# Performance work log

Hardware: AMD Instinct MI355X
Metric: run time of the kernel (lower is better)

The kernel has to match this reference:

```python
import jax, jax.numpy as jnp
import numpy as np

NEG_INF = -1e9  # masked similarity sentinel (cosine sims are in [-1, 1])
EPS = 1e-12     # matches torch F.normalize eps


def _l2norm(x, axis=-1):
    n = jnp.linalg.norm(x, axis=axis, keepdims=True)
    return x / jnp.maximum(n, EPS)


def setup_inputs() -> dict:
    key = jax.random.key(0)
    k1, k2, k3, k4 = jax.random.split(key, 4)
    B, R, D, N = 16, 29, 512, 20000
    query_visual_features = jax.random.normal(k1, (B, R, D), dtype=jnp.float32)
    kb_features = jax.random.normal(k2, (R, N, D), dtype=jnp.float32)
    query_image_ids = jax.random.randint(k3, (B,), 0, 100000)
    kb_image_ids = jax.random.randint(k4, (R, N), 0, 100000)
    return {
        "query_visual_features": query_visual_features,
        "kb_features": kb_features,
        "query_image_ids": query_image_ids,
        "kb_image_ids": kb_image_ids,
        "top_k": 5,
    }


def reference(query_visual_features, kb_features, query_image_ids, kb_image_ids, top_k):
    # Normalize queries (F.normalize dim=2) and KB entries (normalized at init).
    q = _l2norm(query_visual_features)          # [B, R, D]
    kb = _l2norm(kb_features)                   # [R, N, D]
    # Per-sample, per-region cosine similarity against that region's candidates.
    sim = jnp.einsum("brd,rnd->brn", q, kb)    # [B, R, N]
    # Exclude candidates coming from the same image as the query.
    same = kb_image_ids[None, :, :] == query_image_ids[:, None, None]  # [B, R, N]
    sim = jnp.where(same, NEG_INF, sim)
    top_vals, top_idx = jax.lax.top_k(sim, top_k)  # [B, R, k]
    # similarity_scores in the original = best (top-1) similarity per region.
    similarity_scores = top_vals[..., 0]            # [B, R]
    return similarity_scores, top_vals, top_idx
```

## Files before the change

### kernel.cpp

```cpp
#include <hip/hip_runtime.h>
#include <stddef.h>
#include <stdint.h>

#define B_ 16
#define R_ 29
#define D_ 512
#define DF4 128
#define N_ 20000
#define K_ 5
#define TILE 128
#define NTIX ((N_ + TILE - 1) / TILE)
#define NG (NTIX * 4)
#define PCAND (NG * K_)
#define NEG_MASK (-1.0e9f)
#define SENT (-3.0e38f)
#define IXMAX 0x7fffffff

__global__ __launch_bounds__(64) void knorm_kernel(const float* __restrict__ q,
                                                   float* __restrict__ qn) {
    int pair = blockIdx.x;
    int b = pair / R_;
    int r = pair % R_;
    int lane = threadIdx.x;
    const float4* src = (const float4*)(q + ((size_t)(b * R_ + r)) * D_);
    float4 x0 = src[lane * 2];
    float4 x1 = src[lane * 2 + 1];
    float ss = x0.x * x0.x + x0.y * x0.y + x0.z * x0.z + x0.w * x0.w +
               x1.x * x1.x + x1.y * x1.y + x1.z * x1.z + x1.w * x1.w;
#pragma unroll
    for (int off = 32; off; off >>= 1) ss += __shfl_xor(ss, off);
    float inv = 1.0f / fmaxf(sqrtf(ss), 1e-12f);
    float4 y0, y1;
    y0.x = x0.x * inv; y0.y = x0.y * inv; y0.z = x0.z * inv; y0.w = x0.w * inv;
    y1.x = x1.x * inv; y1.y = x1.y * inv; y1.z = x1.z * inv; y1.w = x1.w * inv;
    float4* dst = (float4*)(qn + ((size_t)(r * B_ + b)) * D_);
    dst[lane * 2] = y0;
    dst[lane * 2 + 1] = y1;
}

__global__ __launch_bounds__(256) void ksim_kernel(const float* __restrict__ kb,
                                                   const float* __restrict__ qn,
                                                   const int* __restrict__ qid,
                                                   const int* __restrict__ kbid,
                                                   float* __restrict__ pvals,
                                                   int* __restrict__ pidx) {
    __shared__ float4 qs[B_ * DF4];
    const int r = blockIdx.y;
    const int n0 = blockIdx.x * TILE;
    const int tid = threadIdx.x;

    {
        const float4* src = (const float4*)(qn + (size_t)r * B_ * D_);
#pragma unroll
        for (int i = 0; i < 32; ++i) qs[tid + 256 * i] = src[tid + 256 * i];
    }
    __syncthreads();

    const int w = tid >> 6;
    const int lane = tid & 63;
    const int g = lane >> 3;
    const int s = lane & 7;

    int rowi[4];
    const float4* rowp[4];
    float acc[4][B_];
    float nrm[4];
#pragma unroll
    for (int m = 0; m < 4; ++m) {
        rowi[m] = n0 + w * 32 + g + m * 8;
        int rc = rowi[m] < N_ ? rowi[m] : N_ - 1;
        rowp[m] = (const float4*)(kb + (size_t)r * N_ * D_ + (size_t)rc * D_) + s;
        nrm[m] = 0.0f;
#pragma unroll
        for (int b = 0; b < B_; ++b) acc[m][b] = 0.0f;
    }

    float4 kv[4], kn[4];
#pragma unroll
    for (int m = 0; m < 4; ++m) kv[m] = rowp[m][0];

    for (int p = 0; p < 16; ++p) {
        if (p < 15) {
#pragma unroll
            for (int m = 0; m < 4; ++m) kn[m] = rowp[m][(p + 1) * 8];
        }
#pragma unroll
        for (int m = 0; m < 4; ++m)
            nrm[m] += kv[m].x * kv[m].x + kv[m].y * kv[m].y +
                      kv[m].z * kv[m].z + kv[m].w * kv[m].w;
#pragma unroll
        for (int b = 0; b < B_; ++b) {
            const float4 qv = qs[b * DF4 + p * 8 + s];
#pragma unroll
            for (int m = 0; m < 4; ++m)
                acc[m][b] += kv[m].x * qv.x + kv[m].y * qv.y +
                             kv[m].z * qv.z + kv[m].w * qv.w;
        }
#pragma unroll
        for (int m = 0; m < 4; ++m) kv[m] = kn[m];
    }

#pragma unroll
    for (int m = 0; m < 4; ++m) {
        nrm[m] += __shfl_xor(nrm[m], 1);
        nrm[m] += __shfl_xor(nrm[m], 2);
        nrm[m] += __shfl_xor(nrm[m], 4);
#pragma unroll
        for (int b = 0; b < B_; ++b) {
            acc[m][b] += __shfl_xor(acc[m][b], 1);
            acc[m][b] += __shfl_xor(acc[m][b], 2);
            acc[m][b] += __shfl_xor(acc[m][b], 4);
        }
    }

    float rinv[4];
    int myid[4];
#pragma unroll
    for (int m = 0; m < 4; ++m) {
        rinv[m] = 1.0f / fmaxf(sqrtf(nrm[m]), 1e-12f);
        myid[m] = (rowi[m] < N_) ? kbid[(size_t)r * N_ + rowi[m]] : -1;
    }

    const int group = blockIdx.x * 4 + w;
    for (int b = 0; b < B_; ++b) {
        const int qb = qid[b];
        float v[4];
#pragma unroll
        for (int m = 0; m < 4; ++m) {
            float sv = acc[m][b] * rinv[m];
            if (myid[m] == qb) sv = NEG_MASK;
            if (rowi[m] >= N_) sv = SENT;
            v[m] = sv;
        }
        for (int k = 0; k < K_; ++k) {
            float bv = v[0];
            int bx = rowi[0];
#pragma unroll
            for (int m = 1; m < 4; ++m)
                if (v[m] > bv || (v[m] == bv && rowi[m] < bx)) { bv = v[m]; bx = rowi[m]; }
#pragma unroll
            for (int off = 8; off < 64; off <<= 1) {
                float ov = __shfl_xor(bv, off);
                int ox = __shfl_xor(bx, off);
                if (ov > bv || (ov == bv && ox < bx)) { bv = ov; bx = ox; }
            }
            if (lane == 0) {
                size_t o = (((size_t)r * B_ + b) * NG + group) * K_ + k;
                pvals[o] = bv;
                pidx[o] = bx;
            }
#pragma unroll
            for (int m = 0; m < 4; ++m)
                if (rowi[m] == bx) v[m] = SENT;
        }
    }
}

__global__ __launch_bounds__(64) void ktop_kernel(const float* __restrict__ pvals,
                                                  const int* __restrict__ pidx,
                                                  float* __restrict__ out) {
    int pair = blockIdx.x;
    int b = pair / R_;
    int r = pair % R_;
    int lane = threadIdx.x;
    const float* pv = pvals + ((size_t)r * B_ + b) * PCAND;
    const int* px = pidx + ((size_t)r * B_ + b) * PCAND;

    float tv[5];
    int tx[5];
#pragma unroll
    for (int t = 0; t < 5; ++t) { tv[t] = SENT; tx[t] = IXMAX; }

    for (int j = 0; j < (PCAND + 63) / 64; ++j) {
        int c = lane + 64 * j;
        if (c < PCAND) {
            float v = pv[c];
            int ix = px[c];
            if (v > tv[4] || (v == tv[4] && ix < tx[4])) {
                tv[4] = v; tx[4] = ix;
#pragma unroll
                for (int t = 4; t > 0; --t)
                    if (tv[t] > tv[t - 1] ||
                        (tv[t] == tv[t - 1] && tx[t] < tx[t - 1])) {
                        float fv = tv[t]; tv[t] = tv[t - 1]; tv[t - 1] = fv;
                        int fx = tx[t]; tx[t] = tx[t - 1]; tx[t - 1] = fx;
                    }
            }
        }
    }

#pragma unroll
    for (int k = 0; k < K_; ++k) {
        float bv = tv[0];
        int bx = tx[0];
#pragma unroll
        for (int off = 32; off; off >>= 1) {
            float ov = __shfl_xor(bv, off);
            int ox = __shfl_xor(bx, off);
            if (ov > bv || (ov == bv && ox < bx)) { bv = ov; bx = ox; }
        }
        if (lane == 0) {
            int p = b * R_ + r;
            if (k == 0) out[p] = bv;
            out[B_ * R_ + (size_t)p * K_ + k] = bv;
            out[B_ * R_ + (size_t)B_ * R_ * K_ + (size_t)p * K_ + k] = (float)bx;
        }
        bool f0 = (tx[0] == bx);
        bool f1 = f0 || (tx[1] == bx);
        bool f2 = f1 || (tx[2] == bx);
        bool f3 = f2 || (tx[3] == bx);
        bool f4 = f3 || (tx[4] == bx);
        if (f0) { tv[0] = tv[1]; tx[0] = tx[1]; }
        if (f1) { tv[1] = tv[2]; tx[1] = tx[2]; }
        if (f2) { tv[2] = tv[3]; tx[2] = tx[3]; }
        if (f3) { tv[3] = tv[4]; tx[3] = tx[4]; }
        if (f4) { tv[4] = SENT; tx[4] = IXMAX; }
    }
}

extern "C" void kernel_launch(void* const* d_in, const int* in_sizes, int n_in,
                              void* d_out, int out_size, void* d_ws, size_t ws_size,
                              hipStream_t stream) {
    const float* q    = (const float*)d_in[0];
    const float* kb   = (const float*)d_in[1];
    const int*   qid  = (const int*)d_in[2];
    const int*   kbid = (const int*)d_in[3];
    float* out = (float*)d_out;

    float* qn    = (float*)d_ws;
    float* pvals = qn + (size_t)R_ * B_ * D_;
    int*   pidx  = (int*)(pvals + (size_t)R_ * B_ * NG * K_);

    knorm_kernel<<<B_ * R_, 64, 0, stream>>>(q, qn);
    dim3 g2(NTIX, R_);
    ksim_kernel<<<g2, 256, 0, stream>>>(kb, qn, qid, kbid, pvals, pidx);
    ktop_kernel<<<B_ * R_, 64, 0, stream>>>(pvals, pidx, out);
}
```

Measured before the change: 513.3 us.

## Use 1024-thread blocks with fewer rows per thread and in-block top-k merge

The similarity kernel now runs 1024-thread blocks over 256-row tiles. Each thread handles 2 KB rows instead of 4, and the explicit register double-buffered prefetch is dropped in favour of more resident waves to hide load latency. Per-wave top-5 candidates are merged through shared memory (reusing the query buffer) into one top-5 per block and query. This cuts partial output writes and the work in the final top-k kernel. The launch_bounds(1024, 8) hint asks for very high occupancy, which could squeeze registers hard and cause spills, and the 32KB of LDS per block may limit how many blocks can be resident.

```diff
diff --git a/kernel.cpp b/kernel.cpp
--- a/kernel.cpp
+++ b/kernel.cpp
@@ -8,10 +8,9 @@
 #define DF4 128
 #define N_ 20000
 #define K_ 5
-#define TILE 128
+#define TILE 256
 #define NTIX ((N_ + TILE - 1) / TILE)
-#define NG (NTIX * 4)
-#define PCAND (NG * K_)
+#define PCAND (NTIX * K_)
 #define NEG_MASK (-1.0e9f)
 #define SENT (-3.0e38f)
 #define IXMAX 0x7fffffff
@@ -38,12 +37,12 @@
     dst[lane * 2 + 1] = y1;
 }
 
-__global__ __launch_bounds__(256) void ksim_kernel(const float* __restrict__ kb,
-                                                   const float* __restrict__ qn,
-                                                   const int* __restrict__ qid,
-                                                   const int* __restrict__ kbid,
-                                                   float* __restrict__ pvals,
-                                                   int* __restrict__ pidx) {
+__global__ __launch_bounds__(1024, 8) void ksim_kernel(const float* __restrict__ kb,
+                                                       const float* __restrict__ qn,
+                                                       const int* __restrict__ qid,
+                                                       const int* __restrict__ kbid,
+                                                       float* __restrict__ pvals,
+                                                       int* __restrict__ pidx) {
     __shared__ float4 qs[B_ * DF4];
     const int r = blockIdx.y;
     const int n0 = blockIdx.x * TILE;
@@ -52,7 +51,7 @@
     {
         const float4* src = (const float4*)(qn + (size_t)r * B_ * D_);
 #pragma unroll
-        for (int i = 0; i < 32; ++i) qs[tid + 256 * i] = src[tid + 256 * i];
+        for (int i = 0; i < 8; ++i) qs[tid + 1024 * i] = src[tid + 1024 * i];
     }
     __syncthreads();
 
@@ -61,47 +60,41 @@
     const int g = lane >> 3;
     const int s = lane & 7;
 
-    int rowi[4];
-    const float4* rowp[4];
-    float acc[4][B_];
-    float nrm[4];
-#pragma unroll
-    for (int m = 0; m < 4; ++m) {
-        rowi[m] = n0 + w * 32 + g + m * 8;
+    const char* kbb = (const char*)(kb + (size_t)r * N_ * D_);
+    int rowi[2];
+    unsigned off[2];
+#pragma unroll
+    for (int m = 0; m < 2; ++m) {
+        rowi[m] = n0 + w * 16 + g + m * 8;
         int rc = rowi[m] < N_ ? rowi[m] : N_ - 1;
-        rowp[m] = (const float4*)(kb + (size_t)r * N_ * D_ + (size_t)rc * D_) + s;
+        off[m] = ((unsigned)rc * D_ + s * 4) * 4u;
+    }
+
+    float acc[2][B_];
+    float nrm[2];
+#pragma unroll
+    for (int m = 0; m < 2; ++m) {
         nrm[m] = 0.0f;
 #pragma unroll
         for (int b = 0; b < B_; ++b) acc[m][b] = 0.0f;
     }
 
-    float4 kv[4], kn[4];
-#pragma unroll
-    for (int m = 0; m < 4; ++m) kv[m] = rowp[m][0];
-
+#pragma unroll 4
     for (int p = 0; p < 16; ++p) {
-        if (p < 15) {
-#pragma unroll
-            for (int m = 0; m < 4; ++m) kn[m] = rowp[m][(p + 1) * 8];
-        }
-#pragma unroll
-        for (int m = 0; m < 4; ++m)
-            nrm[m] += kv[m].x * kv[m].x + kv[m].y * kv[m].y +
-                      kv[m].z * kv[m].z + kv[m].w * kv[m].w;
+        float4 kv0 = *(const float4*)(kbb + off[0] + (unsigned)(p * 128));
+        float4 kv1 = *(const float4*)(kbb + off[1] + (unsigned)(p * 128));
+        nrm[0] += kv0.x * kv0.x + kv0.y * kv0.y + kv0.z * kv0.z + kv0.w * kv0.w;
+        nrm[1] += kv1.x * kv1.x + kv1.y * kv1.y + kv1.z * kv1.z + kv1.w * kv1.w;
 #pragma unroll
         for (int b = 0; b < B_; ++b) {
             const float4 qv = qs[b * DF4 + p * 8 + s];
-#pragma unroll
-            for (int m = 0; m < 4; ++m)
-                acc[m][b] += kv[m].x * qv.x + kv[m].y * qv.y +
-                             kv[m].z * qv.z + kv[m].w * qv.w;
-        }
-#pragma unroll
-        for (int m = 0; m < 4; ++m) kv[m] = kn[m];
-    }
-
-#pragma unroll
-    for (int m = 0; m < 4; ++m) {
+            acc[0][b] += kv0.x * qv.x + kv0.y * qv.y + kv0.z * qv.z + kv0.w * qv.w;
+            acc[1][b] += kv1.x * qv.x + kv1.y * qv.y + kv1.z * qv.z + kv1.w * qv.w;
+        }
+    }
+
+#pragma unroll
+    for (int m = 0; m < 2; ++m) {
         nrm[m] += __shfl_xor(nrm[m], 1);
         nrm[m] += __shfl_xor(nrm[m], 2);
         nrm[m] += __shfl_xor(nrm[m], 4);
@@ -113,20 +106,23 @@
         }
     }
 
-    float rinv[4];
-    int myid[4];
-#pragma unroll
-    for (int m = 0; m < 4; ++m) {
+    float rinv[2];
+    int myid[2];
+#pragma unroll
+    for (int m = 0; m < 2; ++m) {
         rinv[m] = 1.0f / fmaxf(sqrtf(nrm[m]), 1e-12f);
         myid[m] = (rowi[m] < N_) ? kbid[(size_t)r * N_ + rowi[m]] : -1;
     }
 
-    const int group = blockIdx.x * 4 + w;
+    __syncthreads();
+    float* vbuf = (float*)qs;
+    int* ibuf = (int*)qs + B_ * 16 * K_;
+
     for (int b = 0; b < B_; ++b) {
         const int qb = qid[b];
-        float v[4];
-#pragma unroll
-        for (int m = 0; m < 4; ++m) {
+        float v[2];
+#pragma unroll
+        for (int m = 0; m < 2; ++m) {
             float sv = acc[m][b] * rinv[m];
             if (myid[m] == qb) sv = NEG_MASK;
             if (rowi[m] >= N_) sv = SENT;
@@ -135,23 +131,47 @@
         for (int k = 0; k < K_; ++k) {
             float bv = v[0];
             int bx = rowi[0];
-#pragma unroll
-            for (int m = 1; m < 4; ++m)
-                if (v[m] > bv || (v[m] == bv && rowi[m] < bx)) { bv = v[m]; bx = rowi[m]; }
-#pragma unroll
-            for (int off = 8; off < 64; off <<= 1) {
-                float ov = __shfl_xor(bv, off);
-                int ox = __shfl_xor(bx, off);
+            if (v[1] > bv || (v[1] == bv && rowi[1] < bx)) { bv = v[1]; bx = rowi[1]; }
+#pragma unroll
+            for (int off2 = 8; off2 < 64; off2 <<= 1) {
+                float ov = __shfl_xor(bv, off2);
+                int ox = __shfl_xor(bx, off2);
                 if (ov > bv || (ov == bv && ox < bx)) { bv = ov; bx = ox; }
             }
             if (lane == 0) {
-                size_t o = (((size_t)r * B_ + b) * NG + group) * K_ + k;
+                vbuf[(b * 16 + w) * K_ + k] = bv;
+                ibuf[(b * 16 + w) * K_ + k] = bx;
+            }
+#pragma unroll
+            for (int m = 0; m < 2; ++m)
+                if (rowi[m] == bx) v[m] = SENT;
+        }
+    }
+    __syncthreads();
+
+    {
+        const int b = w;
+        float v0 = SENT, v1 = SENT;
+        int i0 = IXMAX, i1 = IXMAX;
+        if (lane < 80) { v0 = vbuf[b * 80 + lane]; i0 = ibuf[b * 80 + lane]; }
+        if (lane < 16) { v1 = vbuf[b * 80 + 64 + lane]; i1 = ibuf[b * 80 + 64 + lane]; }
+        for (int k = 0; k < K_; ++k) {
+            float bv = v0;
+            int bx = i0;
+            if (v1 > bv || (v1 == bv && i1 < bx)) { bv = v1; bx = i1; }
+#pragma unroll
+            for (int off2 = 1; off2 < 64; off2 <<= 1) {
+                float ov = __shfl_xor(bv, off2);
+                int ox = __shfl_xor(bx, off2);
+                if (ov > bv || (ov == bv && ox < bx)) { bv = ov; bx = ox; }
+            }
+            if (lane == 0) {
+                size_t o = (((size_t)r * B_ + b) * NTIX + blockIdx.x) * K_ + k;
                 pvals[o] = bv;
                 pidx[o] = bx;
             }
-#pragma unroll
-            for (int m = 0; m < 4; ++m)
-                if (rowi[m] == bx) v[m] = SENT;
+            if (i0 == bx) v0 = SENT;
+            if (i1 == bx) v1 = SENT;
         }
     }
 }
@@ -229,10 +249,10 @@
 
     float* qn    = (float*)d_ws;
     float* pvals = qn + (size_t)R_ * B_ * D_;
-    int*   pidx  = (int*)(pvals + (size_t)R_ * B_ * NG * K_);
+    int*   pidx  = (int*)(pvals + (size_t)R_ * B_ * PCAND);
 
     knorm_kernel<<<B_ * R_, 64, 0, stream>>>(q, qn);
     dim3 g2(NTIX, R_);
-    ksim_kernel<<<g2, 256, 0, stream>>>(kb, qn, qid, kbid, pvals, pidx);
+    ksim_kernel<<<g2, 1024, 0, stream>>>(kb, qn, qid, kbid, pvals, pidx);
     ktop_kernel<<<B_ * R_, 64, 0, stream>>>(pvals, pidx, out);
 }
```

After: 793.8 us. +54.7%, slower.

## Persistent similarity kernel with double-buffered LDS staging and running top-k

Applied to the files above, without the earlier changes.

Replaces the one-block-per-tile similarity kernel with a persistent grid of 256 blocks. Each block walks a contiguous range of (region, 32-row) tiles and stages KB rows into double-buffered LDS through global_load_lds so the next tile's load overlaps compute. Each wave keeps 4 query vectors in registers and maintains a running per-lane top-5, reduced across the wave only when the region changes. This cuts the partial-candidate count and ktop work, at the cost of a partial-buffer init kernel and fewer blocks for hiding memory latency. Each tile now loads 32 rows and only 4 queries per wave, so there is less reuse per loaded row than before.

```diff
diff --git a/kernel.cpp b/kernel.cpp
--- a/kernel.cpp
+++ b/kernel.cpp
@@ -5,13 +5,14 @@
 #define B_ 16
 #define R_ 29
 #define D_ 512
-#define DF4 128
 #define N_ 20000
 #define K_ 5
-#define TILE 128
-#define NTIX ((N_ + TILE - 1) / TILE)
-#define NG (NTIX * 4)
-#define PCAND (NG * K_)
+#define TROWS 32
+#define NTIX (N_ / TROWS)
+#define NTILES (R_ * NTIX)
+#define GRID2 256
+#define SLOTS GRID2
+#define PCAND (SLOTS * K_)
 #define NEG_MASK (-1.0e9f)
 #define SENT (-3.0e38f)
 #define IXMAX 0x7fffffff
@@ -38,122 +39,194 @@
     dst[lane * 2 + 1] = y1;
 }
 
+__global__ __launch_bounds__(256) void kinit_kernel(float* __restrict__ pvals,
+                                                    int total) {
+    int i = blockIdx.x * 256 + threadIdx.x;
+    if (i < total) pvals[i] = SENT;
+}
+
 __global__ __launch_bounds__(256) void ksim_kernel(const float* __restrict__ kb,
                                                    const float* __restrict__ qn,
                                                    const int* __restrict__ qid,
                                                    const int* __restrict__ kbid,
                                                    float* __restrict__ pvals,
                                                    int* __restrict__ pidx) {
-    __shared__ float4 qs[B_ * DF4];
-    const int r = blockIdx.y;
-    const int n0 = blockIdx.x * TILE;
+    __shared__ float4 kbt[2][TROWS * 128];
     const int tid = threadIdx.x;
-
-    {
-        const float4* src = (const float4*)(qn + (size_t)r * B_ * D_);
-#pragma unroll
-        for (int i = 0; i < 32; ++i) qs[tid + 256 * i] = src[tid + 256 * i];
-    }
-    __syncthreads();
-
     const int w = tid >> 6;
     const int lane = tid & 63;
     const int g = lane >> 3;
     const int s = lane & 7;
-
-    int rowi[4];
-    const float4* rowp[4];
-    float acc[4][B_];
-    float nrm[4];
-#pragma unroll
-    for (int m = 0; m < 4; ++m) {
-        rowi[m] = n0 + w * 32 + g + m * 8;
-        int rc = rowi[m] < N_ ? rowi[m] : N_ - 1;
-        rowp[m] = (const float4*)(kb + (size_t)r * N_ * D_ + (size_t)rc * D_) + s;
-        nrm[m] = 0.0f;
-#pragma unroll
-        for (int b = 0; b < B_; ++b) acc[m][b] = 0.0f;
+    const int bid = blockIdx.x;
+
+    const int t0 = (int)(((long long)bid * NTILES) / GRID2);
+    const int t1 = (int)(((long long)(bid + 1) * NTILES) / GRID2);
+
+    float4 qreg[4][16];
+    float tv[4][K_];
+    int tx[4][K_];
+    int qb[4];
+    int cur_r = -1;
+    int buf = 0;
+
+#define STAGE(tix_, bp_) do {                                                  \
+    const float* rb_ = kb + ((size_t)cur_r * N_ +                              \
+                             (size_t)(tix_) * TROWS + (size_t)(w * 8)) * D_;   \
+    char* db_ = (char*)(&kbt[(bp_)][0]) + w * 16384;                           \
+    _Pragma("unroll")                                                          \
+    for (int j_ = 0; j_ < 16; ++j_) {                                          \
+        const float* sp_ = rb_ + (j_ >> 1) * D_ + (j_ & 1) * 256 + lane * 4;   \
+        __builtin_amdgcn_global_load_lds(                                      \
+            (const __attribute__((address_space(1))) void*)sp_,                \
+            (__attribute__((address_space(3))) void*)                          \
+                (db_ + (j_ >> 1) * 2048 + (j_ & 1) * 1024), 16, 0, 0);         \
+    }                                                                          \
+} while (0)
+
+#define EMIT(rr_) do {                                                         \
+    _Pragma("unroll")                                                          \
+    for (int bi_ = 0; bi_ < 4; ++bi_) {                                        \
+        for (int k_ = 0; k_ < K_; ++k_) {                                      \
+            float bv_ = tv[bi_][0];                                            \
+            int bx_ = tx[bi_][0];                                              \
+            _Pragma("unroll")                                                  \
+            for (int of_ = 1; of_ < 64; of_ <<= 1) {                           \
+                float ov_ = __shfl_xor(bv_, of_);                              \
+                int ox_ = __shfl_xor(bx_, of_);                                \
+                if (ov_ > bv_ || (ov_ == bv_ && ox_ < bx_)) { bv_ = ov_; bx_ = ox_; } \
+            }                                                                  \
+            if (lane == 0) {                                                   \
+                size_t o_ = (((size_t)(rr_) * B_ + (w * 4 + bi_)) * SLOTS + bid) * K_ + k_; \
+                pvals[o_] = bv_;                                               \
+                pidx[o_] = bx_;                                                \
+            }                                                                  \
+            bool f0_ = (tx[bi_][0] == bx_);                                    \
+            bool f1_ = f0_ || (tx[bi_][1] == bx_);                             \
+            bool f2_ = f1_ || (tx[bi_][2] == bx_);                             \
+            bool f3_ = f2_ || (tx[bi_][3] == bx_);                             \
+            bool f4_ = f3_ || (tx[bi_][4] == bx_);                             \
+            if (f0_) { tv[bi_][0] = tv[bi_][1]; tx[bi_][0] = tx[bi_][1]; }     \
+            if (f1_) { tv[bi_][1] = tv[bi_][2]; tx[bi_][1] = tx[bi_][2]; }     \
+            if (f2_) { tv[bi_][2] = tv[bi_][3]; tx[bi_][2] = tx[bi_][3]; }     \
+            if (f3_) { tv[bi_][3] = tv[bi_][4]; tx[bi_][3] = tx[bi_][4]; }     \
+            if (f4_) { tv[bi_][4] = SENT; tx[bi_][4] = IXMAX; }                \
+        }                                                                      \
+    }                                                                          \
+} while (0)
+
+    for (int ti = t0; ti < t1; ++ti) {
+        const int r = ti / NTIX;
+        const int tix = ti % NTIX;
+        const int n0 = tix * TROWS;
+
+        if (r != cur_r) {
+            if (cur_r >= 0) EMIT(cur_r);
+#pragma unroll
+            for (int bi = 0; bi < 4; ++bi) {
+#pragma unroll
+                for (int t = 0; t < K_; ++t) { tv[bi][t] = SENT; tx[bi][t] = IXMAX; }
+            }
+            const float* qrb = qn + (size_t)r * B_ * D_;
+#pragma unroll
+            for (int bi = 0; bi < 4; ++bi) {
+                qb[bi] = qid[w * 4 + bi];
+#pragma unroll
+                for (int p = 0; p < 16; ++p)
+                    qreg[bi][p] = *(const float4*)(qrb + (w * 4 + bi) * D_ + p * 32 + s * 4);
+            }
+            cur_r = r;
+            STAGE(tix, buf);
+        }
+
+        const bool next_same = (ti + 1 < t1) && ((ti + 1) < (r + 1) * NTIX);
+        if (next_same) {
+            STAGE(tix + 1, buf ^ 1);
+            asm volatile("s_waitcnt vmcnt(16)" ::: "memory");
+        } else {
+            asm volatile("s_waitcnt vmcnt(0)" ::: "memory");
+        }
+        __builtin_amdgcn_s_barrier();
+        __builtin_amdgcn_sched_barrier(0);
+
+        float acc[4][4];
+        float nrm[4];
+#pragma unroll
+        for (int m = 0; m < 4; ++m) {
+            nrm[m] = 0.0f;
+#pragma unroll
+            for (int bi = 0; bi < 4; ++bi) acc[m][bi] = 0.0f;
+        }
+        const float4* kt = &kbt[buf][0];
+#pragma unroll
+        for (int p = 0; p < 16; ++p) {
+            float4 kv[4];
+#pragma unroll
+            for (int m = 0; m < 4; ++m) kv[m] = kt[(g + 8 * m) * 128 + p * 8 + s];
+#pragma unroll
+            for (int m = 0; m < 4; ++m)
+                nrm[m] += kv[m].x * kv[m].x + kv[m].y * kv[m].y +
+                          kv[m].z * kv[m].z + kv[m].w * kv[m].w;
+#pragma unroll
+            for (int bi = 0; bi < 4; ++bi) {
+#pragma unroll
+                for (int m = 0; m < 4; ++m)
+                    acc[m][bi] += kv[m].x * qreg[bi][p].x + kv[m].y * qreg[bi][p].y +
+                                  kv[m].z * qreg[bi][p].z + kv[m].w * qreg[bi][p].w;
+            }
+        }
+
+#pragma unroll
+        for (int m = 0; m < 4; ++m) {
+            nrm[m] += __shfl_xor(nrm[m], 1);
+            nrm[m] += __shfl_xor(nrm[m], 2);
+            nrm[m] += __shfl_xor(nrm[m], 4);
+#pragma unroll
+            for (int bi = 0; bi < 4; ++bi) {
+                acc[m][bi] += __shfl_xor(acc[m][bi], 1);
+                acc[m][bi] += __shfl_xor(acc[m][bi], 2);
+                acc[m][bi] += __shfl_xor(acc[m][bi], 4);
+            }
+        }
+
+#pragma unroll
+        for (int m = 0; m < 4; ++m) {
+            const int row = n0 + g + 8 * m;
+            const float rinv = 1.0f / fmaxf(sqrtf(nrm[m]), 1e-12f);
+            const int myid = kbid[(size_t)r * N_ + row];
+#pragma unroll
+            for (int bi = 0; bi < 4; ++bi) {
+                float v = acc[m][bi] * rinv;
+                if (myid == qb[bi]) v = NEG_MASK;
+                if (v > tv[bi][4] || (v == tv[bi][4] && row < tx[bi][4])) {
+                    tv[bi][4] = v; tx[bi][4] = row;
+                    if (tv[bi][4] > tv[bi][3] || (tv[bi][4] == tv[bi][3] && tx[bi][4] < tx[bi][3])) {
+                        float fv = tv[bi][4]; tv[bi][4] = tv[bi][3]; tv[bi][3] = fv;
+                        int fx = tx[bi][4]; tx[bi][4] = tx[bi][3]; tx[bi][3] = fx;
+                    }
+                    if (tv[bi][3] > tv[bi][2] || (tv[bi][3] == tv[bi][2] && tx[bi][3] < tx[bi][2])) {
+                        float fv = tv[bi][3]; tv[bi][3] = tv[bi][2]; tv[bi][2] = fv;
+                        int fx = tx[bi][3]; tx[bi][3] = tx[bi][2]; tx[bi][2] = fx;
+                    }
+                    if (tv[bi][2] > tv[bi][1] || (tv[bi][2] == tv[bi][1] && tx[bi][2] < tx[bi][1])) {
+                        float fv = tv[bi][2]; tv[bi][2] = tv[bi][1]; tv[bi][1] = fv;
+                        int fx = tx[bi][2]; tx[bi][2] = tx[bi][1]; tx[bi][1] = fx;
+                    }
+                    if (tv[bi][1] > tv[bi][0] || (tv[bi][1] == tv[bi][0] && tx[bi][1] < tx[bi][0])) {
+                        float fv = tv[bi][1]; tv[bi][1] = tv[bi][0]; tv[bi][0] = fv;
+                        int fx = tx[bi][1]; tx[bi][1] = tx[bi][0]; tx[bi][0] = fx;
+                    }
+                }
+            }
+        }
+
+        __builtin_amdgcn_sched_barrier(0);
+        __builtin_amdgcn_s_barrier();
+        buf ^= 1;
     }
-
-    float4 kv[4], kn[4];
-#pragma unroll
-    for (int m = 0; m < 4; ++m) kv[m] = rowp[m][0];
-
-    for (int p = 0; p < 16; ++p) {
-        if (p < 15) {
-#pragma unroll
-            for (int m = 0; m < 4; ++m) kn[m] = rowp[m][(p + 1) * 8];
-        }
-#pragma unroll
-        for (int m = 0; m < 4; ++m)
-            nrm[m] += kv[m].x * kv[m].x + kv[m].y * kv[m].y +
-                      kv[m].z * kv[m].z + kv[m].w * kv[m].w;
-#pragma unroll
-        for (int b = 0; b < B_; ++b) {
-            const float4 qv = qs[b * DF4 + p * 8 + s];
-#pragma unroll
-            for (int m = 0; m < 4; ++m)
-                acc[m][b] += kv[m].x * qv.x + kv[m].y * qv.y +
-                             kv[m].z * qv.z + kv[m].w * qv.w;
-        }
-#pragma unroll
-        for (int m = 0; m < 4; ++m) kv[m] = kn[m];
-    }
-
-#pragma unroll
-    for (int m = 0; m < 4; ++m) {
-        nrm[m] += __shfl_xor(nrm[m], 1);
-        nrm[m] += __shfl_xor(nrm[m], 2);
-        nrm[m] += __shfl_xor(nrm[m], 4);
-#pragma unroll
-        for (int b = 0; b < B_; ++b) {
-            acc[m][b] += __shfl_xor(acc[m][b], 1);
-            acc[m][b] += __shfl_xor(acc[m][b], 2);
-            acc[m][b] += __shfl_xor(acc[m][b], 4);
-        }
-    }
-
-    float rinv[4];
-    int myid[4];
-#pragma unroll
-    for (int m = 0; m < 4; ++m) {
-        rinv[m] = 1.0f / fmaxf(sqrtf(nrm[m]), 1e-12f);
-        myid[m] = (rowi[m] < N_) ? kbid[(size_t)r * N_ + rowi[m]] : -1;
-    }
-
-    const int group = blockIdx.x * 4 + w;
-    for (int b = 0; b < B_; ++b) {
-        const int qb = qid[b];
-        float v[4];
-#pragma unroll
-        for (int m = 0; m < 4; ++m) {
-            float sv = acc[m][b] * rinv[m];
-            if (myid[m] == qb) sv = NEG_MASK;
-            if (rowi[m] >= N_) sv = SENT;
-            v[m] = sv;
-        }
-        for (int k = 0; k < K_; ++k) {
-            float bv = v[0];
-            int bx = rowi[0];
-#pragma unroll
-            for (int m = 1; m < 4; ++m)
-                if (v[m] > bv || (v[m] == bv && rowi[m] < bx)) { bv = v[m]; bx = rowi[m]; }
-#pragma unroll
-            for (int off = 8; off < 64; off <<= 1) {
-                float ov = __shfl_xor(bv, off);
-                int ox = __shfl_xor(bx, off);
-                if (ov > bv || (ov == bv && ox < bx)) { bv = ov; bx = ox; }
-            }
-            if (lane == 0) {
-                size_t o = (((size_t)r * B_ + b) * NG + group) * K_ + k;
-                pvals[o] = bv;
-                pidx[o] = bx;
-            }
-#pragma unroll
-            for (int m = 0; m < 4; ++m)
-                if (rowi[m] == bx) v[m] = SENT;
-        }
-    }
+    if (cur_r >= 0) EMIT(cur_r);
+
+#undef STAGE
+#undef EMIT
 }
 
 __global__ __launch_bounds__(64) void ktop_kernel(const float* __restrict__ pvals,
@@ -171,21 +244,19 @@
 #pragma unroll
     for (int t = 0; t < 5; ++t) { tv[t] = SENT; tx[t] = IXMAX; }
 
-    for (int j = 0; j < (PCAND + 63) / 64; ++j) {
+    for (int j = 0; j < PCAND / 64; ++j) {
         int c = lane + 64 * j;
-        if (c < PCAND) {
-            float v = pv[c];
-            int ix = px[c];
-            if (v > tv[4] || (v == tv[4] && ix < tx[4])) {
-                tv[4] = v; tx[4] = ix;
-#pragma unroll
-                for (int t = 4; t > 0; --t)
-                    if (tv[t] > tv[t - 1] ||
-                        (tv[t] == tv[t - 1] && tx[t] < tx[t - 1])) {
-                        float fv = tv[t]; tv[t] = tv[t - 1]; tv[t - 1] = fv;
-                        int fx = tx[t]; tx[t] = tx[t - 1]; tx[t - 1] = fx;
-                    }
-            }
+        float v = pv[c];
+        int ix = px[c];
+        if (v > tv[4] || (v == tv[4] && ix < tx[4])) {
+            tv[4] = v; tx[4] = ix;
+#pragma unroll
+            for (int t = 4; t > 0; --t)
+                if (tv[t] > tv[t - 1] ||
+                    (tv[t] == tv[t - 1] && tx[t] < tx[t - 1])) {
+                    float fv = tv[t]; tv[t] = tv[t - 1]; tv[t - 1] = fv;
+                    int fx = tx[t]; tx[t] = tx[t - 1]; tx[t - 1] = fx;
+                }
         }
     }
 
@@ -229,10 +300,12 @@
 
     float* qn    = (float*)d_ws;
     float* pvals = qn + (size_t)R_ * B_ * D_;
-    int*   pidx  = (int*)(pvals + (size_t)R_ * B_ * NG * K_);
+    int*   pidx  = (int*)(pvals + (size_t)R_ * B_ * SLOTS * K_);
+
+    const int ptotal = R_ * B_ * SLOTS * K_;
 
     knorm_kernel<<<B_ * R_, 64, 0, stream>>>(q, qn);
-    dim3 g2(NTIX, R_);
-    ksim_kernel<<<g2, 256, 0, stream>>>(kb, qn, qid, kbid, pvals, pidx);
+    kinit_kernel<<<(ptotal + 255) / 256, 256, 0, stream>>>(pvals, ptotal);
+    ksim_kernel<<<GRID2, 256, 0, stream>>>(kb, qn, qid, kbid, pvals, pidx);
     ktop_kernel<<<B_ * R_, 64, 0, stream>>>(pvals, pidx, out);
 }
```

New measurement: 805.2 us. 56.9% more time.
